# Kernel tuning notes

Measured on AMD Instinct MI355X. Metric: run time of the kernel, lower is better.

## Reference

```python
import jax, jax.numpy as jnp
import numpy as np
import math

# ---- real-basis Wigner 3j via nullspace of rotation generators ----

def _su2_gen(l):
    m = np.arange(-l, l + 1)
    jz = np.diag(m).astype(complex)
    jp = np.zeros((2 * l + 1, 2 * l + 1), complex)
    for i, mm in enumerate(m[:-1]):
        jp[i + 1, i] = math.sqrt(l * (l + 1) - mm * (mm + 1))
    jm = jp.conj().T
    return (jp + jm) / 2, (jp - jm) / 2j, jz


def _c2r(l):
    # complex -> real spherical-harmonic change of basis
    U = np.zeros((2 * l + 1, 2 * l + 1), complex)
    U[l, l] = 1.0
    s = 1 / math.sqrt(2)
    for m in range(1, l + 1):
        U[l + m, l + m] = (-1) ** m * s
        U[l + m, l - m] = s
        U[l - m, l - m] = 1j * s
        U[l - m, l + m] = -1j * (-1) ** m * s
    return U


def _real_gens(l):
    U = _c2r(l)
    return [np.real(U @ (-1j * J) @ U.conj().T) for J in _su2_gen(l)]


_W3J_CACHE = {}

def _w3j(l1, l2, l3):
    key = (l1, l2, l3)
    if key in _W3J_CACHE:
        return _W3J_CACHE[key]
    X1, X2, X3 = _real_gens(l1), _real_gens(l2), _real_gens(l3)
    d1, d2, d3 = 2 * l1 + 1, 2 * l2 + 1, 2 * l3 + 1
    I1, I2, I3 = np.eye(d1), np.eye(d2), np.eye(d3)
    blocks = []
    for a in range(3):
        K = (np.kron(np.kron(X1[a], I2), I3)
             + np.kron(np.kron(I1, X2[a]), I3)
             + np.kron(np.kron(I1, I2), X3[a]))
        blocks.append(K)
    M = np.concatenate(blocks, 0)
    _, _, Vh = np.linalg.svd(M)
    v = Vh[-1]
    if v[np.argmax(np.abs(v))] < 0:
        v = -v
    w = (v / np.linalg.norm(v)).reshape(d1, d2, d3)
    _W3J_CACHE[key] = w
    return w


# ---- replicate WeightedTensorProduct.__init__ layout logic ----

def _build(ls1, ls2, ls_out):
    dim = lambda ls: sum(2 * l + 1 for l in ls)
    d1, d2, do = dim(ls1), dim(ls2), dim(ls_out)
    lmax2 = max(ls2)
    max_l3 = max(ls_out) + 1
    layout = {}
    idx1 = 0
    for l1 in ls1:
        idx2 = 0
        for l2 in ls2:
            for l3 in range(abs(l1 - l2), min(l1 + l2 + 1, max_l3)):
                layout.setdefault(l3, []).append((l1, l2, idx1 * d2 + idx2))
            idx2 += 2 * l2 + 1
        idx1 += 2 * l1 + 1
    l3s = sorted(layout)
    cbh = sum((2 * l3 + 1) * len(layout[l3]) for l3 in l3s)
    cb = np.zeros((cbh, d1 * d2), np.float32)
    row = 0
    for l3 in l3s:
        layout[l3] = sorted(layout[l3], key=lambda x: x[0] * lmax2 + x[1])
        for (l1, l2, col) in layout[l3]:
            w = _w3j(l1, l2, l3) * math.sqrt(2 * l3 + 1)  # (2l1+1, 2l2+1, 2l3+1)
            for m1 in range(2 * l1 + 1):
                cb[row:row + 2 * l3 + 1, col + m1 * d2: col + m1 * d2 + 2 * l2 + 1] = w[m1].T
            row += 2 * l3 + 1
    # weight-tying mask (one scalar weight per (out-irrep, cb-path) pair)
    out_mult = {}
    for l in ls_out:
        out_mult[l] = out_mult.get(l, 0) + 1
    rows_idx, cols_idx = [], []
    row_idx, widx = 0, 0
    for ol3 in sorted(out_mult):
        for _ in range(out_mult[ol3]):
            col_idx = 0
            for l3 in l3s:
                for _m in range(len(layout[l3])):
                    if ol3 == l3:
                        for m in range(2 * l3 + 1):
                            rows_idx.append((row_idx + m) * cbh + col_idx + m)
                            cols_idx.append(widx)
                        widx += 1
                    col_idx += 2 * l3 + 1
            row_idx += 2 * ol3 + 1
    return cb, np.array(rows_idx, np.int32), np.array(cols_idx, np.int32), widx, do, cbh


def setup_inputs() -> dict:
    LS = [0] * 8 + [1] * 8 + [2] * 4  # dim = 52, for in1, in2 and out
    cb, rows, cols, nw, do, H = _build(LS, LS, LS)
    d = sum(2 * l + 1 for l in LS)
    rng = np.random.default_rng(0)
    w = rng.standard_normal(nw).astype(np.float32)
    Wf = np.zeros(do * H, np.float32)
    Wf[rows] = w[cols]
    B = 4096
    k1, k2 = jax.random.split(jax.random.key(0))
    return {
        "in1": jax.random.normal(k1, (B, d), jnp.float32),
        "in2": jax.random.normal(k2, (B, d), jnp.float32),
        "cb_matrix": jnp.asarray(cb),                  # [H, d*d]
        "weight_matrix": jnp.asarray(Wf.reshape(do, H)),  # [do, H]
    }


def reference(in1, in2, cb_matrix, weight_matrix):
    # out = (W @ C @ outer^T)^T  ==  outer @ C^T @ W^T
    B = in1.shape[0]
    outer = (in1[:, :, None] * in2[:, None, :]).reshape(B, -1)  # [B, d1*d2]
    z = outer @ cb_matrix.T                                     # [B, cb_height]
    return z @ weight_matrix.T                                  # [B, dim_out]
```

## Files before the change

### kernel.cpp

```cpp
#include <hip/hip_runtime.h>
#include <hip/hip_bf16.h>

#define D    52
#define DD   2704
#define HH   2000
#define DO   52
#define KP   3328
#define NO   64
#define KS   8
#define KT_TOTAL (KP/32)
#define KT_PER   (KT_TOTAL/KS)
#define MG   8
#define KCH  256
#define WHP  2048

typedef __attribute__((ext_vector_type(8))) short short8;
typedef __attribute__((ext_vector_type(4))) float f32x4;

#define WB_OFF     0
#define WB_BYTES   (NO * WHP * 2)
#define MTP_OFF    (WB_OFF + WB_BYTES)
#define MTP_BYTES  (MG * NO * DD * 4)
#define MTB_OFF    (MTP_OFF + MTP_BYTES)
#define MTB_BYTES  (KT_TOTAL * NO * 32 * 2)
#define OUTP_OFF   (MTB_OFF + MTB_BYTES)
#define OUTP_BYTES (KS * 4096 * NO * 4)

static __device__ __forceinline__ unsigned short f2bf(float f) {
    __hip_bfloat16 h = __float2bfloat16(f);
    return __builtin_bit_cast(unsigned short, h);
}

__global__ __launch_bounds__(256) void k_packw(
    const float* __restrict__ W, unsigned short* __restrict__ Wb) {
    int idx = blockIdx.x * 256 + threadIdx.x;
    if (idx >= NO * WHP) return;
    int o = idx >> 11, h = idx & (WHP - 1);
    float v = (o < DO && h < HH) ? W[o * HH + h] : 0.f;
    Wb[idx] = f2bf(v);
}

__global__ __launch_bounds__(256) void k_mgemm(
    const float* __restrict__ cb, const unsigned short* __restrict__ Wb,
    float* __restrict__ mtp) {
    __shared__ float shAT[64][33];
    int lane = threadIdx.x & 63;
    int w    = __builtin_amdgcn_readfirstlane(threadIdx.x >> 6);
    int r    = lane & 15;
    int kg   = lane >> 4;
    int ij0  = blockIdx.x * 64;
    int g    = blockIdx.y;

    f32x4 acc[4];
#pragma unroll
    for (int mt = 0; mt < 4; ++mt) acc[mt] = (f32x4){0.f, 0.f, 0.f, 0.f};

    int srow = threadIdx.x >> 6;
    int scol = threadIdx.x & 63;
    int sij  = ij0 + scol;
    bool ijv = (sij < DD);

#pragma unroll
    for (int kt = 0; kt < KCH / 32; ++kt) {
        int h0 = g * KCH + kt * 32;
        __syncthreads();
#pragma unroll
        for (int p = 0; p < 8; ++p) {
            int row = srow + p * 4;
            int h = h0 + row;
            float v = (h < HH && ijv) ? cb[(size_t)h * DD + sij] : 0.f;
            shAT[scol][row] = v;
        }
        __syncthreads();

        short8 bf;
#pragma unroll
        for (int e = 0; e < 8; ++e)
            bf[e] = (short)f2bf(shAT[w * 16 + r][kg * 8 + e]);
#pragma unroll
        for (int mt = 0; mt < 4; ++mt) {
            short8 a = *reinterpret_cast<const short8*>(
                Wb + (size_t)(mt * 16 + r) * WHP + g * KCH + kt * 32 + kg * 8);
            acc[mt] = __builtin_amdgcn_mfma_f32_16x16x32_bf16(a, bf, acc[mt], 0, 0, 0);
        }
    }

    int ij = ij0 + w * 16 + r;
    if (ij < DD) {
#pragma unroll
        for (int mt = 0; mt < 4; ++mt) {
#pragma unroll
            for (int q = 0; q < 4; ++q) {
                int o = mt * 16 + kg * 4 + q;
                mtp[((size_t)g * NO + o) * DD + ij] = acc[mt][q];
            }
        }
    }
}

__global__ __launch_bounds__(256) void k_reduce_mtb(
    const float* __restrict__ mtp, unsigned short* __restrict__ mtB) {
    int k = blockIdx.x * 256 + threadIdx.x;
    int o = blockIdx.y;
    int i = k >> 6, j = k & 63;
    float s = 0.f;
    if (j < D) {
        size_t base = (size_t)o * DD + i * D + j;
#pragma unroll
        for (int g = 0; g < MG; ++g) s += mtp[(size_t)g * (NO * DD) + base];
    }
    mtB[((size_t)(k >> 5) * NO + o) * 32 + ((k >> 3) & 3) * 8 + (k & 7)] = f2bf(s);
}

__global__ __launch_bounds__(256) void k_main_mfma(
    const float* __restrict__ in1, const float* __restrict__ in2,
    const unsigned short* __restrict__ mtB, float* __restrict__ outp) {
    __shared__ float sh1[64][53];
    __shared__ float sh2[64][72];

    int lane = threadIdx.x & 63;
    int w    = __builtin_amdgcn_readfirstlane(threadIdx.x >> 6);
    int b0   = blockIdx.x * 64;
    int ks   = blockIdx.y;
    int r    = lane & 15;
    int kg   = lane >> 4;

    for (int t = threadIdx.x; t < 64 * 13; t += 256) {
        int row = t / 13, q = t - row * 13;
        float4 v = *reinterpret_cast<const float4*>(in2 + (size_t)(b0 + row) * D + 4 * q);
        sh2[row][4 * q + 0] = v.x; sh2[row][4 * q + 1] = v.y;
        sh2[row][4 * q + 2] = v.z; sh2[row][4 * q + 3] = v.w;
    }
    for (int t = threadIdx.x; t < 64 * 12; t += 256) {
        int row = t / 12, j = 52 + (t - row * 12);
        sh2[row][j] = 0.f;
    }
    for (int t = threadIdx.x; t < 64 * 13; t += 256) {
        int row = t / 13, q = t - row * 13;
        float4 v = *reinterpret_cast<const float4*>(in1 + (size_t)(b0 + row) * D + 4 * q);
        sh1[row][4 * q + 0] = v.x; sh1[row][4 * q + 1] = v.y;
        sh1[row][4 * q + 2] = v.z; sh1[row][4 * q + 3] = v.w;
    }
    __syncthreads();

    int mrow = w * 16 + r;
    f32x4 acc[4];
#pragma unroll
    for (int nt = 0; nt < 4; ++nt) acc[nt] = (f32x4){0.f, 0.f, 0.f, 0.f};

    const unsigned short* bbase =
        mtB + ((size_t)(ks * KT_PER) * NO + r) * 32 + kg * 8;

#pragma unroll 4
    for (int t = 0; t < KT_PER; ++t) {
        int kt   = ks * KT_PER + t;
        int i    = kt >> 1;
        int j0   = (kt & 1) * 32 + kg * 8;
        float f1 = sh1[mrow][i];
        float4 v0 = *reinterpret_cast<const float4*>(&sh2[mrow][j0]);
        float4 v1 = *reinterpret_cast<const float4*>(&sh2[mrow][j0 + 4]);
        short8 a;
        a[0] = (short)f2bf(f1 * v0.x); a[1] = (short)f2bf(f1 * v0.y);
        a[2] = (short)f2bf(f1 * v0.z); a[3] = (short)f2bf(f1 * v0.w);
        a[4] = (short)f2bf(f1 * v1.x); a[5] = (short)f2bf(f1 * v1.y);
        a[6] = (short)f2bf(f1 * v1.z); a[7] = (short)f2bf(f1 * v1.w);
#pragma unroll
        for (int nt = 0; nt < 4; ++nt) {
            short8 b = *reinterpret_cast<const short8*>(
                bbase + ((size_t)t * NO + nt * 16) * 32);
            acc[nt] = __builtin_amdgcn_mfma_f32_16x16x32_bf16(a, b, acc[nt], 0, 0, 0);
        }
    }

#pragma unroll
    for (int nt = 0; nt < 4; ++nt) {
#pragma unroll
        for (int q = 0; q < 4; ++q) {
            outp[((size_t)ks * 4096 + b0 + w * 16 + kg * 4 + q) * NO + nt * 16 + r]
                = acc[nt][q];
        }
    }
}

__global__ __launch_bounds__(256) void k_out(
    const float* __restrict__ outp, float* __restrict__ out, int B) {
    int idx = blockIdx.x * 256 + threadIdx.x;
    if (idx >= B * DO) return;
    int b = idx / DO, o = idx - b * DO;
    float s = 0.f;
#pragma unroll
    for (int g = 0; g < KS; ++g) s += outp[((size_t)g * B + b) * NO + o];
    out[idx] = s;
}

extern "C" void kernel_launch(void* const* d_in, const int* in_sizes, int n_in,
                              void* d_out, int out_size, void* d_ws, size_t ws_size,
                              hipStream_t stream) {
    const float* in1 = (const float*)d_in[0];
    const float* in2 = (const float*)d_in[1];
    const float* cb  = (const float*)d_in[2];
    const float* W   = (const float*)d_in[3];
    float* out = (float*)d_out;

    int B = in_sizes[0] / D;

    char* ws = (char*)d_ws;
    unsigned short* Wb   = (unsigned short*)(ws + WB_OFF);
    float*          mtp  = (float*)(ws + MTP_OFF);
    unsigned short* mtB  = (unsigned short*)(ws + MTB_OFF);
    float*          outp = (float*)(ws + OUTP_OFF);

    hipLaunchKernelGGL(k_packw, dim3((NO * WHP + 255) / 256), dim3(256), 0,
                       stream, W, Wb);
    hipLaunchKernelGGL(k_mgemm, dim3((DD + 63) / 64, MG), dim3(256), 0,
                       stream, cb, Wb, mtp);
    hipLaunchKernelGGL(k_reduce_mtb, dim3(KP / 256, NO), dim3(256), 0,
                       stream, mtp, mtB);
    hipLaunchKernelGGL(k_main_mfma, dim3(B / 64, KS), dim3(256), 0,
                       stream, in1, in2, mtB, outp);
    hipLaunchKernelGGL(k_out, dim3((B * DO + 255) / 256), dim3(256), 0,
                       stream, outp, out, B);
}
```

Before: 114.7 us.

## Fuse split-K reduction into main MFMA kernel via in-block LDS reduction

The main GEMM now runs 16 batch rows per 512-thread block, with each of the 8 waves taking one K slice. Partial results are reduced in shared memory and written straight to the output, so the separate k_out kernel and its global partial buffer go away. The M-GEMM K-split also changes from 8 chunks of 256 to 16 chunks of 128, giving more blocks but more partials for the reduce kernel to sum. Each block now reads the full mtB matrix for only 16 rows, which raises the amount of B-operand traffic sent through L2.

```diff
diff --git a/kernel.cpp b/kernel.cpp
--- a/kernel.cpp
+++ b/kernel.cpp
@@ -7,11 +7,10 @@
 #define DO   52
 #define KP   3328
 #define NO   64
-#define KS   8
 #define KT_TOTAL (KP/32)
-#define KT_PER   (KT_TOTAL/KS)
-#define MG   8
-#define KCH  256
+#define KT_W   (KT_TOTAL/8)
+#define MG   16
+#define KCH  128
 #define WHP  2048
 
 typedef __attribute__((ext_vector_type(8))) short short8;
@@ -23,8 +22,6 @@
 #define MTP_BYTES  (MG * NO * DD * 4)
 #define MTB_OFF    (MTP_OFF + MTP_BYTES)
 #define MTB_BYTES  (KT_TOTAL * NO * 32 * 2)
-#define OUTP_OFF   (MTB_OFF + MTB_BYTES)
-#define OUTP_BYTES (KS * 4096 * NO * 4)
 
 static __device__ __forceinline__ unsigned short f2bf(float f) {
     __hip_bfloat16 h = __float2bfloat16(f);
@@ -112,30 +109,31 @@
     mtB[((size_t)(k >> 5) * NO + o) * 32 + ((k >> 3) & 3) * 8 + (k & 7)] = f2bf(s);
 }
 
-__global__ __launch_bounds__(256) void k_main_mfma(
+__global__ __launch_bounds__(512) void k_main_fused(
     const float* __restrict__ in1, const float* __restrict__ in2,
-    const unsigned short* __restrict__ mtB, float* __restrict__ outp) {
-    __shared__ float sh1[64][53];
-    __shared__ float sh2[64][72];
-
-    int lane = threadIdx.x & 63;
-    int w    = __builtin_amdgcn_readfirstlane(threadIdx.x >> 6);
-    int b0   = blockIdx.x * 64;
-    int ks   = blockIdx.y;
+    const unsigned short* __restrict__ mtB, float* __restrict__ out) {
+    __shared__ float sh1[16][53];
+    __shared__ float sh2[16][72];
+    __shared__ float red[8][16][64];
+
+    int tid  = threadIdx.x;
+    int lane = tid & 63;
+    int w    = __builtin_amdgcn_readfirstlane(tid >> 6);
     int r    = lane & 15;
     int kg   = lane >> 4;
-
-    for (int t = threadIdx.x; t < 64 * 13; t += 256) {
+    int b0   = blockIdx.x * 16;
+
+    for (int t = tid; t < 16 * 13; t += 512) {
         int row = t / 13, q = t - row * 13;
         float4 v = *reinterpret_cast<const float4*>(in2 + (size_t)(b0 + row) * D + 4 * q);
         sh2[row][4 * q + 0] = v.x; sh2[row][4 * q + 1] = v.y;
         sh2[row][4 * q + 2] = v.z; sh2[row][4 * q + 3] = v.w;
     }
-    for (int t = threadIdx.x; t < 64 * 12; t += 256) {
+    for (int t = tid; t < 16 * 12; t += 512) {
         int row = t / 12, j = 52 + (t - row * 12);
         sh2[row][j] = 0.f;
     }
-    for (int t = threadIdx.x; t < 64 * 13; t += 256) {
+    for (int t = tid; t < 16 * 13; t += 512) {
         int row = t / 13, q = t - row * 13;
         float4 v = *reinterpret_cast<const float4*>(in1 + (size_t)(b0 + row) * D + 4 * q);
         sh1[row][4 * q + 0] = v.x; sh1[row][4 * q + 1] = v.y;
@@ -143,22 +141,21 @@
     }
     __syncthreads();
 
-    int mrow = w * 16 + r;
     f32x4 acc[4];
 #pragma unroll
     for (int nt = 0; nt < 4; ++nt) acc[nt] = (f32x4){0.f, 0.f, 0.f, 0.f};
 
     const unsigned short* bbase =
-        mtB + ((size_t)(ks * KT_PER) * NO + r) * 32 + kg * 8;
-
-#pragma unroll 4
-    for (int t = 0; t < KT_PER; ++t) {
-        int kt   = ks * KT_PER + t;
+        mtB + ((size_t)(w * KT_W) * NO + r) * 32 + kg * 8;
+
+#pragma unroll
+    for (int t = 0; t < KT_W; ++t) {
+        int kt   = w * KT_W + t;
         int i    = kt >> 1;
         int j0   = (kt & 1) * 32 + kg * 8;
-        float f1 = sh1[mrow][i];
-        float4 v0 = *reinterpret_cast<const float4*>(&sh2[mrow][j0]);
-        float4 v1 = *reinterpret_cast<const float4*>(&sh2[mrow][j0 + 4]);
+        float f1 = sh1[r][i];
+        float4 v0 = *reinterpret_cast<const float4*>(&sh2[r][j0]);
+        float4 v1 = *reinterpret_cast<const float4*>(&sh2[r][j0 + 4]);
         short8 a;
         a[0] = (short)f2bf(f1 * v0.x); a[1] = (short)f2bf(f1 * v0.y);
         a[2] = (short)f2bf(f1 * v0.z); a[3] = (short)f2bf(f1 * v0.w);
@@ -176,21 +173,18 @@
     for (int nt = 0; nt < 4; ++nt) {
 #pragma unroll
         for (int q = 0; q < 4; ++q) {
-            outp[((size_t)ks * 4096 + b0 + w * 16 + kg * 4 + q) * NO + nt * 16 + r]
-                = acc[nt][q];
-        }
-    }
-}
-
-__global__ __launch_bounds__(256) void k_out(
-    const float* __restrict__ outp, float* __restrict__ out, int B) {
-    int idx = blockIdx.x * 256 + threadIdx.x;
-    if (idx >= B * DO) return;
-    int b = idx / DO, o = idx - b * DO;
-    float s = 0.f;
-#pragma unroll
-    for (int g = 0; g < KS; ++g) s += outp[((size_t)g * B + b) * NO + o];
-    out[idx] = s;
+            red[w][kg * 4 + q][nt * 16 + r] = acc[nt][q];
+        }
+    }
+    __syncthreads();
+
+    for (int idx = tid; idx < 16 * 64; idx += 512) {
+        int row = idx >> 6, o = idx & 63;
+        float s = 0.f;
+#pragma unroll
+        for (int ww = 0; ww < 8; ++ww) s += red[ww][row][o];
+        if (o < DO) out[(size_t)(b0 + row) * DO + o] = s;
+    }
 }
 
 extern "C" void kernel_launch(void* const* d_in, const int* in_sizes, int n_in,
@@ -205,10 +199,9 @@
     int B = in_sizes[0] / D;
 
     char* ws = (char*)d_ws;
-    unsigned short* Wb   = (unsigned short*)(ws + WB_OFF);
-    float*          mtp  = (float*)(ws + MTP_OFF);
-    unsigned short* mtB  = (unsigned short*)(ws + MTB_OFF);
-    float*          outp = (float*)(ws + OUTP_OFF);
+    unsigned short* Wb  = (unsigned short*)(ws + WB_OFF);
+    float*          mtp = (float*)(ws + MTP_OFF);
+    unsigned short* mtB = (unsigned short*)(ws + MTB_OFF);
 
     hipLaunchKernelGGL(k_packw, dim3((NO * WHP + 255) / 256), dim3(256), 0,
                        stream, W, Wb);
@@ -216,8 +209,6 @@
                        stream, cb, Wb, mtp);
     hipLaunchKernelGGL(k_reduce_mtb, dim3(KP / 256, NO), dim3(256), 0,
                        stream, mtp, mtB);
-    hipLaunchKernelGGL(k_main_mfma, dim3(B / 64, KS), dim3(256), 0,
-                       stream, in1, in2, mtB, outp);
-    hipLaunchKernelGGL(k_out, dim3((B * DO + 255) / 256), dim3(256), 0,
-                       stream, outp, out, B);
-}
+    hipLaunchKernelGGL(k_main_fused, dim3(B / 16), dim3(512), 0,
+                       stream, in1, in2, mtB, out);
+}
```

Measured after the change: 101.2 us (median of 2 runs). 1.13x faster.
